# Optimization experiments

Hardware: AMD Instinct MI355X
Metric: run time of the kernel (lower is better)

The kernel has to match this reference:

```python
import jax, jax.numpy as jnp
import numpy as np


def setup_inputs() -> dict:
    key = jax.random.key(0)
    embeddings = jax.random.normal(key, (4, 2048, 128), dtype=jnp.float32)
    return {"embeddings": embeddings}


def _pairwise_dist(x):
    # x: [N, D] -> Euclidean distance matrix [N, N] (matches torch.cdist, p=2)
    sq = jnp.sum(x * x, axis=-1)  # [N]
    d2 = sq[:, None] + sq[None, :] - 2.0 * (x @ x.T)
    d2 = jnp.maximum(d2, 0.0)
    # safe sqrt: exact 0 on the diagonal / coincident points, no NaN grads
    safe = jnp.where(d2 > 0.0, d2, 1.0)
    return jnp.where(d2 > 0.0, jnp.sqrt(safe), 0.0)


def reference(embeddings) -> jnp.ndarray:
    b, s, d = embeddings.shape
    x = embeddings.reshape(b * s, d)
    dist = _pairwise_dist(x)                 # [N, N]
    mean_dist = jnp.mean(dist)
    # torch.std default: unbiased (ddof=1) over all elements
    std_dist = jnp.std(dist, ddof=1)
    return std_dist / (mean_dist + 1e-08)
```

## Files before the change

### kernel.cpp

```cpp
#include <hip/hip_runtime.h>
#include <hip/hip_bf16.h>
#include <math.h>


#define NPTS   8192
#define DIM    128
#define BT     256
#define NT2    (NPTS / BT)
#define NBLK   (NT2 * (NT2 + 1) / 2)
#define NPREP  (NPTS / 32)
#define NTILES (NPTS / 128)
#define NTOTSQ (NTILES * NTILES)

typedef __attribute__((ext_vector_type(8))) short short8;
typedef __attribute__((ext_vector_type(4))) float f32x4;

typedef const __attribute__((address_space(1))) void* gas_ptr;
typedef __attribute__((address_space(3))) void* las_ptr;

__device__ __forceinline__ void gload16(const void* g, void* l) {
    __builtin_amdgcn_global_load_lds((gas_ptr)g, (las_ptr)l, 16, 0, 0);
}
__device__ __forceinline__ float fsqrt(float x) {
    return __builtin_amdgcn_sqrtf(x);
}

__global__ __launch_bounds__(256)
void ph_prep(const float* __restrict__ x, ushort* __restrict__ xb,
             float* __restrict__ sq, float* __restrict__ cs_part)
{
    __shared__ float xs[32][129];
    const int tid = threadIdx.x;
    const int rw  = tid >> 3;
    const int row = blockIdx.x * 32 + rw;
    const int seg = tid & 7;
    const float4* p = reinterpret_cast<const float4*>(x + (size_t)row * DIM + seg * 16);
    float v[16];
    {
        float4 a = p[0], b = p[1], c = p[2], d = p[3];
        v[0]=a.x; v[1]=a.y; v[2]=a.z; v[3]=a.w;  v[4]=b.x; v[5]=b.y; v[6]=b.z; v[7]=b.w;
        v[8]=c.x; v[9]=c.y; v[10]=c.z; v[11]=c.w; v[12]=d.x; v[13]=d.y; v[14]=d.z; v[15]=d.w;
    }
    float s = 0.f;
    ushort h[16];
#pragma unroll
    for (int j = 0; j < 16; ++j) {
        __hip_bfloat16 hb = __float2bfloat16(v[j]);
        h[j] = *reinterpret_cast<ushort*>(&hb);
        s = fmaf(v[j], v[j], s);
        xs[rw][seg * 16 + j] = v[j];
    }
    short8 o0, o1;
#pragma unroll
    for (int j = 0; j < 8; ++j) { o0[j] = (short)h[j]; o1[j] = (short)h[j+8]; }
    short8* dst = reinterpret_cast<short8*>(xb + (size_t)row * DIM + seg * 16);
    dst[0] = o0; dst[1] = o1;
    s += __shfl_xor(s, 1); s += __shfl_xor(s, 2); s += __shfl_xor(s, 4);
    if (seg == 0) sq[row] = s;
    __syncthreads();
    if (tid < DIM) {
        float c = 0.f;
#pragma unroll 8
        for (int r = 0; r < 32; ++r) c += xs[r][tid];
        cs_part[blockIdx.x * DIM + tid] = c;
    }
}

__global__ __launch_bounds__(1024, 4)
void ph_gram(const ushort* __restrict__ xb, const float* __restrict__ sq,
             double* __restrict__ partials)
{
    const int f   = blockIdx.x;
    const int tid = threadIdx.x;

    int bi = (int)((65.0f - fsqrt((float)(4225 - 8 * f))) * 0.5f);
    while ((bi + 1) * 32 - ((bi + 1) * bi) / 2 <= f) ++bi;
    while (bi * 32 - (bi * (bi - 1)) / 2 > f) --bi;
    const int bj = bi + (f - (bi * 32 - (bi * (bi - 1)) / 2));

    __shared__ ushort A0[BT * 64], B0[BT * 64];
    __shared__ ushort A1[BT * 64], B1[BT * 64];
    __shared__ double rr[32];

    const int lane = tid & 63;
    const int wv   = tid >> 6;
    const int wr   = wv >> 2;
    const int wc   = wv & 3;

    const char* gA = (const char*)(xb + (size_t)bi * BT * DIM);
    const char* gB = (const char*)(xb + (size_t)bj * BT * DIM);

    const bool  stA  = wv < 8;
    const char* gsrc = stA ? gA : gB;
    const int   c0   = (wv & 7) * 4;
    const int   srow = lane >> 3;
    const int   skb  = (lane & 7) * 16;

#define STAGE(h, dA, dB)                                                      \
    {                                                                         \
        char* dst_ = stA ? (char*)(dA) : (char*)(dB);                         \
        _Pragma("unroll")                                                     \
        for (int c = 0; c < 4; ++c) {                                         \
            const int chunk = c0 + c;                                         \
            const int row   = chunk * 8 + srow;                               \
            const size_t go = (size_t)row * 256 + (h) * 128                   \
                              + (skb ^ ((row & 7) << 4));                     \
            gload16(gsrc + go, dst_ + chunk * 1024);                          \
        }                                                                     \
    }

    f32x4 acc[4][4];
#pragma unroll
    for (int m = 0; m < 4; ++m)
#pragma unroll
        for (int n = 0; n < 4; ++n) acc[m][n] = (f32x4){0.f, 0.f, 0.f, 0.f};

#define COMPUTE(dA, dB)                                                       \
    {                                                                         \
        _Pragma("unroll")                                                     \
        for (int ks = 0; ks < 2; ++ks) {                                      \
            const int kb = ks * 64 + (lane >> 4) * 16;                        \
            short8 af[4], bfr[4];                                             \
            _Pragma("unroll")                                                 \
            for (int m = 0; m < 4; ++m) {                                     \
                const int row = wr * 64 + m * 16 + (lane & 15);               \
                af[m] = *reinterpret_cast<const short8*>(                     \
                    (const char*)(dA) + row * 128 + (kb ^ ((row & 7) << 4))); \
            }                                                                 \
            _Pragma("unroll")                                                 \
            for (int n = 0; n < 4; ++n) {                                     \
                const int col = wc * 64 + n * 16 + (lane & 15);               \
                bfr[n] = *reinterpret_cast<const short8*>(                    \
                    (const char*)(dB) + col * 128 + (kb ^ ((col & 7) << 4))); \
            }                                                                 \
            __builtin_amdgcn_s_setprio(1);                                    \
            _Pragma("unroll")                                                 \
            for (int m = 0; m < 4; ++m)                                       \
                _Pragma("unroll")                                             \
                for (int n = 0; n < 4; ++n)                                   \
                    acc[m][n] = __builtin_amdgcn_mfma_f32_16x16x32_bf16(      \
                        af[m], bfr[n], acc[m][n], 0, 0, 0);                   \
            __builtin_amdgcn_s_setprio(0);                                    \
        }                                                                     \
    }

    STAGE(0, A0, B0);
    __syncthreads();
    STAGE(1, A1, B1);
    COMPUTE(A0, B0);
    __syncthreads();
    COMPUTE(A1, B1);

    const float* sqA = sq + bi * BT + wr * 64 + (lane >> 4) * 4;
    const float* sqB = sq + bj * BT + wc * 64 + (lane & 15);
    float nb[4];
#pragma unroll
    for (int n = 0; n < 4; ++n) nb[n] = sqB[n * 16];

    float s1a = 0.f, s1b = 0.f, s1c = 0.f, s1d = 0.f;
    const bool diag = (bi == bj);
    if (!diag) {
#pragma unroll
        for (int m = 0; m < 4; ++m) {
            const float4 v = *reinterpret_cast<const float4*>(sqA + m * 16);
#pragma unroll
            for (int n = 0; n < 4; ++n) {
                s1a += fsqrt(fmaxf(fmaf(-2.f, acc[m][n][0], v.x + nb[n]), 0.f));
                s1b += fsqrt(fmaxf(fmaf(-2.f, acc[m][n][1], v.y + nb[n]), 0.f));
                s1c += fsqrt(fmaxf(fmaf(-2.f, acc[m][n][2], v.z + nb[n]), 0.f));
                s1d += fsqrt(fmaxf(fmaf(-2.f, acc[m][n][3], v.w + nb[n]), 0.f));
            }
        }
    } else {
#pragma unroll
        for (int m = 0; m < 4; ++m) {
            const float4 v = *reinterpret_cast<const float4*>(sqA + m * 16);
            const float nav[4] = {v.x, v.y, v.z, v.w};
#pragma unroll
            for (int n = 0; n < 4; ++n) {
                const int col = wc * 64 + n * 16 + (lane & 15);
#pragma unroll
                for (int r = 0; r < 4; ++r) {
                    const int row = wr * 64 + m * 16 + (lane >> 4) * 4 + r;
                    float d = fmaxf(fmaf(-2.f, acc[m][n][r], nav[r] + nb[n]), 0.f);
                    if (row == col) d = 0.f;
                    s1a += fsqrt(d);
                }
            }
        }
    }
    float s1 = (s1a + s1b) + (s1c + s1d);
#pragma unroll
    for (int off = 1; off < 64; off <<= 1) s1 += __shfl_xor(s1, off);
    const double w = diag ? 1.0 : 2.0;
    if (lane == 0) rr[wv] = (double)s1 * w;
    __syncthreads();
    if (tid == 0) {
        double t1 = 0.0;
#pragma unroll
        for (int i = 0; i < 16; ++i) t1 += rr[i];
        partials[f] = t1;
    }
#undef STAGE
#undef COMPUTE
}

__global__ __launch_bounds__(256)
void ph_finalize(const double* __restrict__ partials, const float* __restrict__ sq,
                 const float* __restrict__ cs_part, float* __restrict__ out)
{
    __shared__ double r1[256], r2[256], r3[128];
    const int tid = threadIdx.x;
    double s1 = 0.0;
    for (int i = tid; i < NBLK; i += 256) s1 += partials[i];
    double sn = 0.0;
    for (int k = 0; k < NPTS / 256; ++k) sn += (double)sq[tid + k * 256];
    r1[tid] = s1; r2[tid] = sn;
    if (tid < DIM) {
        double c = 0.0;
        for (int b = 0; b < NPREP; ++b) c += (double)cs_part[b * DIM + tid];
        r3[tid] = c * c;
    }
    __syncthreads();
    for (int off = 128; off > 0; off >>= 1) {
        if (tid < off) { r1[tid] += r1[tid + off]; r2[tid] += r2[tid + off]; }
        __syncthreads();
    }
    for (int off = 64; off > 0; off >>= 1) {
        if (tid < off) r3[tid] += r3[tid + off];
        __syncthreads();
    }
    if (tid == 0) {
        const double M    = (double)NPTS * (double)NPTS;
        const double S1   = r1[0];
        const double S2   = 2.0 * (double)NPTS * r2[0] - 2.0 * r3[0];
        const double mean = S1 / M;
        double var = (S2 - S1 * S1 / M) / (M - 1.0);
        if (var < 0.0) var = 0.0;
        out[0] = (float)(sqrt(var) / (mean + 1e-8));
    }
}

#define LSTR 132
__global__ __launch_bounds__(256)
void ph_pair_kernel(const float* __restrict__ x, double* __restrict__ partials)
{
    const int bi  = blockIdx.y;
    const int bj  = blockIdx.x;
    const int tid = threadIdx.x;
    const int flat = bi * NTILES + bj;
    if (bj < bi) {
        if (tid == 0) { partials[2*flat] = 0.0; partials[2*flat+1] = 0.0; }
        return;
    }
    __shared__ __align__(16) float As[128 * LSTR];
    __shared__ __align__(16) float Bs[128 * LSTR];
    __shared__ float  nA[128];
    __shared__ float  nB[128];
    __shared__ double red1[256];
    __shared__ double red2[256];
    const float* Ab = x + (size_t)bi * 128 * DIM;
    const float* Bb = x + (size_t)bj * 128 * DIM;
#pragma unroll
    for (int it = 0; it < 16; ++it) {
        const int e   = (tid + it * 256) * 4;
        const int row = e >> 7;
        const int k   = e & 127;
        float4 va = *reinterpret_cast<const float4*>(Ab + e);
        As[(k+0)*LSTR + row] = va.x; As[(k+1)*LSTR + row] = va.y;
        As[(k+2)*LSTR + row] = va.z; As[(k+3)*LSTR + row] = va.w;
        float4 vb = *reinterpret_cast<const float4*>(Bb + e);
        Bs[(k+0)*LSTR + row] = vb.x; Bs[(k+1)*LSTR + row] = vb.y;
        Bs[(k+2)*LSTR + row] = vb.z; Bs[(k+3)*LSTR + row] = vb.w;
    }
    __syncthreads();
    if (tid < 128) {
        float s = 0.f;
#pragma unroll 8
        for (int k = 0; k < DIM; ++k) { float v = As[k*LSTR + tid]; s = fmaf(v, v, s); }
        nA[tid] = s;
    } else {
        const int r = tid - 128;
        float s = 0.f;
#pragma unroll 8
        for (int k = 0; k < DIM; ++k) { float v = Bs[k*LSTR + r]; s = fmaf(v, v, s); }
        nB[r] = s;
    }
    __syncthreads();
    const int tx = tid & 15, ty = tid >> 4;
    const int ra = ty * 8, cb = tx * 8;
    float acc[8][8];
#pragma unroll
    for (int r = 0; r < 8; ++r)
#pragma unroll
        for (int c = 0; c < 8; ++c) acc[r][c] = 0.f;
#pragma unroll 4
    for (int k = 0; k < DIM; ++k) {
        const float4 a0 = *reinterpret_cast<const float4*>(&As[k*LSTR + ra]);
        const float4 a1 = *reinterpret_cast<const float4*>(&As[k*LSTR + ra + 4]);
        const float4 b0 = *reinterpret_cast<const float4*>(&Bs[k*LSTR + cb]);
        const float4 b1 = *reinterpret_cast<const float4*>(&Bs[k*LSTR + cb + 4]);
        const float a[8] = {a0.x,a0.y,a0.z,a0.w,a1.x,a1.y,a1.z,a1.w};
        const float b[8] = {b0.x,b0.y,b0.z,b0.w,b1.x,b1.y,b1.z,b1.w};
#pragma unroll
        for (int r = 0; r < 8; ++r)
#pragma unroll
            for (int c = 0; c < 8; ++c)
                acc[r][c] = fmaf(a[r], b[c], acc[r][c]);
    }
    double s1 = 0.0, s2 = 0.0;
    const int gi0 = bi*128 + ra, gj0 = bj*128 + cb;
#pragma unroll
    for (int r = 0; r < 8; ++r) {
#pragma unroll
        for (int c = 0; c < 8; ++c) {
            float d2 = nA[ra+r] + nB[cb+c] - 2.0f * acc[r][c];
            d2 = fmaxf(d2, 0.0f);
            if (gi0 + r == gj0 + c) d2 = 0.0f;
            s1 += (double)sqrtf(d2);
            s2 += (double)d2;
        }
    }
    const double w = (bi == bj) ? 1.0 : 2.0;
    s1 *= w; s2 *= w;
    red1[tid] = s1; red2[tid] = s2;
    __syncthreads();
    for (int off = 128; off > 0; off >>= 1) {
        if (tid < off) { red1[tid] += red1[tid+off]; red2[tid] += red2[tid+off]; }
        __syncthreads();
    }
    if (tid == 0) { partials[2*flat] = red1[0]; partials[2*flat+1] = red2[0]; }
}

__global__ __launch_bounds__(256)
void ph_finalize_sq(const double* __restrict__ partials, float* __restrict__ out)
{
    __shared__ double r1[256], r2[256];
    const int tid = threadIdx.x;
    double s1 = 0.0, s2 = 0.0;
    for (int i = tid; i < NTOTSQ; i += 256) { s1 += partials[2*i]; s2 += partials[2*i+1]; }
    r1[tid] = s1; r2[tid] = s2;
    __syncthreads();
    for (int off = 128; off > 0; off >>= 1) {
        if (tid < off) { r1[tid] += r1[tid+off]; r2[tid] += r2[tid+off]; }
        __syncthreads();
    }
    if (tid == 0) {
        const double M    = (double)NPTS * (double)NPTS;
        const double mean = r1[0] / M;
        double var = (r2[0] - r1[0]*r1[0]/M) / (M - 1.0);
        if (var < 0.0) var = 0.0;
        out[0] = (float)(sqrt(var) / (mean + 1e-8));
    }
}

extern "C" void kernel_launch(void* const* d_in, const int* in_sizes, int n_in,
                              void* d_out, int out_size, void* d_ws, size_t ws_size,
                              hipStream_t stream)
{
    const float* x = (const float*)d_in[0];
    float* out     = (float*)d_out;

    const size_t XB_OFF = 0;
    const size_t SQ_OFF = (size_t)NPTS * DIM * sizeof(ushort);
    const size_t CS_OFF = SQ_OFF + NPTS * sizeof(float);
    const size_t PT_OFF = CS_OFF + (size_t)NPREP * DIM * sizeof(float);
    const size_t NEEDED = PT_OFF + (size_t)NBLK * sizeof(double);

    if (ws_size >= NEEDED) {
        ushort* xb       = (ushort*)((char*)d_ws + XB_OFF);
        float*  sq       = (float*) ((char*)d_ws + SQ_OFF);
        float*  cs_part  = (float*) ((char*)d_ws + CS_OFF);
        double* partials = (double*)((char*)d_ws + PT_OFF);

        ph_prep<<<NPREP, 256, 0, stream>>>(x, xb, sq, cs_part);
        ph_gram<<<NBLK, 1024, 0, stream>>>(xb, sq, partials);
        ph_finalize<<<1, 256, 0, stream>>>(partials, sq, cs_part, out);
    } else {
        double* partials = (double*)d_ws;
        ph_pair_kernel<<<dim3(NTILES, NTILES), 256, 0, stream>>>(x, partials);
        ph_finalize_sq<<<1, 256, 0, stream>>>(partials, out);
    }
}
```

Before: 38.35 us.

## Shrink Gram tiles to 128x128 with 256-thread blocks and single-buffered LDS

Changes the upper-triangular Gram tile from 256x256 with 1024 threads to 128x128 with 256 threads. The grid grows from 528 to 2080 blocks, and LDS per block falls from four 32KB buffers to two 16KB buffers. Staging is no longer double-buffered: each K-half is loaded, synced and computed in sequence. The aim is better occupancy and load balance across CUs, at the cost of more redundant global loads per flop and exposed load latency.

```diff
diff --git a/kernel.cpp b/kernel.cpp
--- a/kernel.cpp
+++ b/kernel.cpp
@@ -5,9 +5,9 @@
 
 #define NPTS   8192
 #define DIM    128
-#define BT     256
-#define NT2    (NPTS / BT)
-#define NBLK   (NT2 * (NT2 + 1) / 2)
+#define TIL    128
+#define NGRID  (NPTS / TIL)
+#define NTOT   (NGRID * (NGRID + 1) / 2)
 #define NPREP  (NPTS / 32)
 #define NTILES (NPTS / 128)
 #define NTOTSQ (NTILES * NTILES)
@@ -66,46 +66,43 @@
     }
 }
 
-__global__ __launch_bounds__(1024, 4)
+__global__ __launch_bounds__(256, 4)
 void ph_gram(const ushort* __restrict__ xb, const float* __restrict__ sq,
              double* __restrict__ partials)
 {
     const int f   = blockIdx.x;
     const int tid = threadIdx.x;
 
-    int bi = (int)((65.0f - fsqrt((float)(4225 - 8 * f))) * 0.5f);
-    while ((bi + 1) * 32 - ((bi + 1) * bi) / 2 <= f) ++bi;
-    while (bi * 32 - (bi * (bi - 1)) / 2 > f) --bi;
-    const int bj = bi + (f - (bi * 32 - (bi * (bi - 1)) / 2));
-
-    __shared__ ushort A0[BT * 64], B0[BT * 64];
-    __shared__ ushort A1[BT * 64], B1[BT * 64];
-    __shared__ double rr[32];
+    int bi = (int)((129.0f - fsqrt((float)(16641 - 8 * f))) * 0.5f);
+    while ((bi + 1) * 64 - ((bi + 1) * bi) / 2 <= f) ++bi;
+    while (bi * 64 - (bi * (bi - 1)) / 2 > f) --bi;
+    const int bj = bi + (f - (bi * 64 - (bi * (bi - 1)) / 2));
+
+    __shared__ ushort Ah[TIL * 64];
+    __shared__ ushort Bh[TIL * 64];
+    __shared__ double rr[4];
 
     const int lane = tid & 63;
     const int wv   = tid >> 6;
-    const int wr   = wv >> 2;
-    const int wc   = wv & 3;
-
-    const char* gA = (const char*)(xb + (size_t)bi * BT * DIM);
-    const char* gB = (const char*)(xb + (size_t)bj * BT * DIM);
-
-    const bool  stA  = wv < 8;
-    const char* gsrc = stA ? gA : gB;
-    const int   c0   = (wv & 7) * 4;
-    const int   srow = lane >> 3;
-    const int   skb  = (lane & 7) * 16;
-
-#define STAGE(h, dA, dB)                                                      \
+    const int wr   = wv >> 1;
+    const int wc   = wv & 1;
+
+    const char* gA = (const char*)(xb + (size_t)bi * TIL * DIM);
+    const char* gB = (const char*)(xb + (size_t)bj * TIL * DIM);
+
+    const int srow = lane >> 3;
+    const int skb  = (lane & 7) * 16;
+
+#define STAGE(h)                                                              \
     {                                                                         \
-        char* dst_ = stA ? (char*)(dA) : (char*)(dB);                         \
         _Pragma("unroll")                                                     \
         for (int c = 0; c < 4; ++c) {                                         \
-            const int chunk = c0 + c;                                         \
+            const int chunk = wv * 4 + c;                                     \
             const int row   = chunk * 8 + srow;                               \
             const size_t go = (size_t)row * 256 + (h) * 128                   \
                               + (skb ^ ((row & 7) << 4));                     \
-            gload16(gsrc + go, dst_ + chunk * 1024);                          \
+            gload16(gA + go, (char*)Ah + chunk * 1024);                       \
+            gload16(gB + go, (char*)Bh + chunk * 1024);                       \
         }                                                                     \
     }
 
@@ -115,7 +112,7 @@
 #pragma unroll
         for (int n = 0; n < 4; ++n) acc[m][n] = (f32x4){0.f, 0.f, 0.f, 0.f};
 
-#define COMPUTE(dA, dB)                                                       \
+#define COMPUTE()                                                             \
     {                                                                         \
         _Pragma("unroll")                                                     \
         for (int ks = 0; ks < 2; ++ks) {                                      \
@@ -125,13 +122,13 @@
             for (int m = 0; m < 4; ++m) {                                     \
                 const int row = wr * 64 + m * 16 + (lane & 15);               \
                 af[m] = *reinterpret_cast<const short8*>(                     \
-                    (const char*)(dA) + row * 128 + (kb ^ ((row & 7) << 4))); \
+                    (const char*)Ah + row * 128 + (kb ^ ((row & 7) << 4)));   \
             }                                                                 \
             _Pragma("unroll")                                                 \
             for (int n = 0; n < 4; ++n) {                                     \
                 const int col = wc * 64 + n * 16 + (lane & 15);               \
                 bfr[n] = *reinterpret_cast<const short8*>(                    \
-                    (const char*)(dB) + col * 128 + (kb ^ ((col & 7) << 4))); \
+                    (const char*)Bh + col * 128 + (kb ^ ((col & 7) << 4)));   \
             }                                                                 \
             __builtin_amdgcn_s_setprio(1);                                    \
             _Pragma("unroll")                                                 \
@@ -144,15 +141,16 @@
         }                                                                     \
     }
 
-    STAGE(0, A0, B0);
-    __syncthreads();
-    STAGE(1, A1, B1);
-    COMPUTE(A0, B0);
-    __syncthreads();
-    COMPUTE(A1, B1);
-
-    const float* sqA = sq + bi * BT + wr * 64 + (lane >> 4) * 4;
-    const float* sqB = sq + bj * BT + wc * 64 + (lane & 15);
+    STAGE(0);
+    __syncthreads();
+    COMPUTE();
+    __syncthreads();
+    STAGE(1);
+    __syncthreads();
+    COMPUTE();
+
+    const float* sqA = sq + bi * TIL + wr * 64 + (lane >> 4) * 4;
+    const float* sqB = sq + bj * TIL + wc * 64 + (lane & 15);
     float nb[4];
 #pragma unroll
     for (int n = 0; n < 4; ++n) nb[n] = sqB[n * 16];
@@ -195,12 +193,7 @@
     const double w = diag ? 1.0 : 2.0;
     if (lane == 0) rr[wv] = (double)s1 * w;
     __syncthreads();
-    if (tid == 0) {
-        double t1 = 0.0;
-#pragma unroll
-        for (int i = 0; i < 16; ++i) t1 += rr[i];
-        partials[f] = t1;
-    }
+    if (tid == 0) partials[f] = (rr[0] + rr[1]) + (rr[2] + rr[3]);
 #undef STAGE
 #undef COMPUTE
 }
@@ -212,7 +205,7 @@
     __shared__ double r1[256], r2[256], r3[128];
     const int tid = threadIdx.x;
     double s1 = 0.0;
-    for (int i = tid; i < NBLK; i += 256) s1 += partials[i];
+    for (int i = tid; i < NTOT; i += 256) s1 += partials[i];
     double sn = 0.0;
     for (int k = 0; k < NPTS / 256; ++k) sn += (double)sq[tid + k * 256];
     r1[tid] = s1; r2[tid] = sn;
@@ -365,7 +358,7 @@
     const size_t SQ_OFF = (size_t)NPTS * DIM * sizeof(ushort);
     const size_t CS_OFF = SQ_OFF + NPTS * sizeof(float);
     const size_t PT_OFF = CS_OFF + (size_t)NPREP * DIM * sizeof(float);
-    const size_t NEEDED = PT_OFF + (size_t)NBLK * sizeof(double);
+    const size_t NEEDED = PT_OFF + (size_t)NTOT * sizeof(double);
 
     if (ws_size >= NEEDED) {
         ushort* xb       = (ushort*)((char*)d_ws + XB_OFF);
@@ -374,7 +367,7 @@
         double* partials = (double*)((char*)d_ws + PT_OFF);
 
         ph_prep<<<NPREP, 256, 0, stream>>>(x, xb, sq, cs_part);
-        ph_gram<<<NBLK, 1024, 0, stream>>>(xb, sq, partials);
+        ph_gram<<<NTOT, 256, 0, stream>>>(xb, sq, partials);
         ph_finalize<<<1, 256, 0, stream>>>(partials, sq, cs_part, out);
     } else {
         double* partials = (double*)d_ws;
```

Result: faster. 35.47 us (-7.5%).

## Fuse finalize into gram kernel via last-block atomic counter; use 512-thread blocks

Applied to the files above, without the earlier changes.

Removes the separate finalize kernel launch. The last gram block to finish, found through an atomic counter that the prep kernel resets, now does the final reductions. The gram kernel also drops from 1024 to 512 threads, so each wave computes a 128x64 sub-tile with twice as many accumulators, and the setprio hints are removed. This saves one launch and its gap but raises register pressure per wave and serialises the final reduction on a single block.

```diff
diff --git a/kernel.cpp b/kernel.cpp
--- a/kernel.cpp
+++ b/kernel.cpp
@@ -27,10 +27,12 @@
 
 __global__ __launch_bounds__(256)
 void ph_prep(const float* __restrict__ x, ushort* __restrict__ xb,
-             float* __restrict__ sq, float* __restrict__ cs_part)
+             float* __restrict__ sq, float* __restrict__ cs_part,
+             unsigned int* __restrict__ counter)
 {
     __shared__ float xs[32][129];
     const int tid = threadIdx.x;
+    if (blockIdx.x == 0 && tid == 0) counter[0] = 0u;
     const int rw  = tid >> 3;
     const int row = blockIdx.x * 32 + rw;
     const int seg = tid & 7;
@@ -66,9 +68,10 @@
     }
 }
 
-__global__ __launch_bounds__(1024, 4)
+__global__ __launch_bounds__(512)
 void ph_gram(const ushort* __restrict__ xb, const float* __restrict__ sq,
-             double* __restrict__ partials)
+             const float* __restrict__ cs_part, double* __restrict__ partials,
+             unsigned int* __restrict__ counter, float* __restrict__ out)
 {
     const int f   = blockIdx.x;
     const int tid = threadIdx.x;
@@ -80,19 +83,21 @@
 
     __shared__ ushort A0[BT * 64], B0[BT * 64];
     __shared__ ushort A1[BT * 64], B1[BT * 64];
-    __shared__ double rr[32];
+    __shared__ double rr[16];
+    __shared__ double red[512];
+    __shared__ int    lastFlag;
 
     const int lane = tid & 63;
     const int wv   = tid >> 6;
-    const int wr   = wv >> 2;
-    const int wc   = wv & 3;
+    const int wr2  = wv >> 2;
+    const int wc4  = wv & 3;
 
     const char* gA = (const char*)(xb + (size_t)bi * BT * DIM);
     const char* gB = (const char*)(xb + (size_t)bj * BT * DIM);
 
-    const bool  stA  = wv < 8;
+    const bool  stA  = wv < 4;
     const char* gsrc = stA ? gA : gB;
-    const int   c0   = (wv & 7) * 4;
+    const int   cb0  = (wv & 3) * 8;
     const int   srow = lane >> 3;
     const int   skb  = (lane & 7) * 16;
 
@@ -100,8 +105,8 @@
     {                                                                         \
         char* dst_ = stA ? (char*)(dA) : (char*)(dB);                         \
         _Pragma("unroll")                                                     \
-        for (int c = 0; c < 4; ++c) {                                         \
-            const int chunk = c0 + c;                                         \
+        for (int c = 0; c < 8; ++c) {                                         \
+            const int chunk = cb0 + c;                                        \
             const int row   = chunk * 8 + srow;                               \
             const size_t go = (size_t)row * 256 + (h) * 128                   \
                               + (skb ^ ((row & 7) << 4));                     \
@@ -109,9 +114,9 @@
         }                                                                     \
     }
 
-    f32x4 acc[4][4];
-#pragma unroll
-    for (int m = 0; m < 4; ++m)
+    f32x4 acc[8][4];
+#pragma unroll
+    for (int m = 0; m < 8; ++m)
 #pragma unroll
         for (int n = 0; n < 4; ++n) acc[m][n] = (f32x4){0.f, 0.f, 0.f, 0.f};
 
@@ -120,27 +125,25 @@
         _Pragma("unroll")                                                     \
         for (int ks = 0; ks < 2; ++ks) {                                      \
             const int kb = ks * 64 + (lane >> 4) * 16;                        \
-            short8 af[4], bfr[4];                                             \
+            short8 af[8], bfr[4];                                             \
             _Pragma("unroll")                                                 \
-            for (int m = 0; m < 4; ++m) {                                     \
-                const int row = wr * 64 + m * 16 + (lane & 15);               \
+            for (int m = 0; m < 8; ++m) {                                     \
+                const int row = wr2 * 128 + m * 16 + (lane & 15);             \
                 af[m] = *reinterpret_cast<const short8*>(                     \
                     (const char*)(dA) + row * 128 + (kb ^ ((row & 7) << 4))); \
             }                                                                 \
             _Pragma("unroll")                                                 \
             for (int n = 0; n < 4; ++n) {                                     \
-                const int col = wc * 64 + n * 16 + (lane & 15);               \
+                const int col = wc4 * 64 + n * 16 + (lane & 15);              \
                 bfr[n] = *reinterpret_cast<const short8*>(                    \
                     (const char*)(dB) + col * 128 + (kb ^ ((col & 7) << 4))); \
             }                                                                 \
-            __builtin_amdgcn_s_setprio(1);                                    \
             _Pragma("unroll")                                                 \
-            for (int m = 0; m < 4; ++m)                                       \
+            for (int m = 0; m < 8; ++m)                                       \
                 _Pragma("unroll")                                             \
                 for (int n = 0; n < 4; ++n)                                   \
                     acc[m][n] = __builtin_amdgcn_mfma_f32_16x16x32_bf16(      \
                         af[m], bfr[n], acc[m][n], 0, 0, 0);                   \
-            __builtin_amdgcn_s_setprio(0);                                    \
         }                                                                     \
     }
 
@@ -151,8 +154,8 @@
     __syncthreads();
     COMPUTE(A1, B1);
 
-    const float* sqA = sq + bi * BT + wr * 64 + (lane >> 4) * 4;
-    const float* sqB = sq + bj * BT + wc * 64 + (lane & 15);
+    const float* sqA = sq + bi * BT + wr2 * 128 + (lane >> 4) * 4;
+    const float* sqB = sq + bj * BT + wc4 * 64 + (lane & 15);
     float nb[4];
 #pragma unroll
     for (int n = 0; n < 4; ++n) nb[n] = sqB[n * 16];
@@ -161,7 +164,7 @@
     const bool diag = (bi == bj);
     if (!diag) {
 #pragma unroll
-        for (int m = 0; m < 4; ++m) {
+        for (int m = 0; m < 8; ++m) {
             const float4 v = *reinterpret_cast<const float4*>(sqA + m * 16);
 #pragma unroll
             for (int n = 0; n < 4; ++n) {
@@ -173,15 +176,15 @@
         }
     } else {
 #pragma unroll
-        for (int m = 0; m < 4; ++m) {
+        for (int m = 0; m < 8; ++m) {
             const float4 v = *reinterpret_cast<const float4*>(sqA + m * 16);
             const float nav[4] = {v.x, v.y, v.z, v.w};
 #pragma unroll
             for (int n = 0; n < 4; ++n) {
-                const int col = wc * 64 + n * 16 + (lane & 15);
+                const int col = wc4 * 64 + n * 16 + (lane & 15);
 #pragma unroll
                 for (int r = 0; r < 4; ++r) {
-                    const int row = wr * 64 + m * 16 + (lane >> 4) * 4 + r;
+                    const int row = wr2 * 128 + m * 16 + (lane >> 4) * 4 + r;
                     float d = fmaxf(fmaf(-2.f, acc[m][n][r], nav[r] + nb[n]), 0.f);
                     if (row == col) d = 0.f;
                     s1a += fsqrt(d);
@@ -198,47 +201,60 @@
     if (tid == 0) {
         double t1 = 0.0;
 #pragma unroll
-        for (int i = 0; i < 16; ++i) t1 += rr[i];
+        for (int i = 0; i < 8; ++i) t1 += rr[i];
         partials[f] = t1;
     }
-#undef STAGE
-#undef COMPUTE
-}
-
-__global__ __launch_bounds__(256)
-void ph_finalize(const double* __restrict__ partials, const float* __restrict__ sq,
-                 const float* __restrict__ cs_part, float* __restrict__ out)
-{
-    __shared__ double r1[256], r2[256], r3[128];
-    const int tid = threadIdx.x;
-    double s1 = 0.0;
-    for (int i = tid; i < NBLK; i += 256) s1 += partials[i];
-    double sn = 0.0;
-    for (int k = 0; k < NPTS / 256; ++k) sn += (double)sq[tid + k * 256];
-    r1[tid] = s1; r2[tid] = sn;
+
+    __threadfence();
+    if (tid == 0) {
+        unsigned int prev = atomicAdd(counter, 1u);
+        lastFlag = (prev == (unsigned int)(NBLK - 1));
+    }
+    __syncthreads();
+    if (!lastFlag) return;
+    __threadfence();
+
+    double t = 0.0;
+    for (int i = tid; i < NBLK; i += 512) t += partials[i];
+    red[tid] = t; __syncthreads();
+    for (int off = 256; off > 0; off >>= 1) {
+        if (tid < off) red[tid] += red[tid + off];
+        __syncthreads();
+    }
+    const double S1 = red[0];
+    __syncthreads();
+
+    t = 0.0;
+    for (int i = tid; i < NPTS; i += 512) t += (double)sq[i];
+    red[tid] = t; __syncthreads();
+    for (int off = 256; off > 0; off >>= 1) {
+        if (tid < off) red[tid] += red[tid + off];
+        __syncthreads();
+    }
+    const double SN = red[0];
+    __syncthreads();
+
+    t = 0.0;
     if (tid < DIM) {
         double c = 0.0;
         for (int b = 0; b < NPREP; ++b) c += (double)cs_part[b * DIM + tid];
-        r3[tid] = c * c;
-    }
-    __syncthreads();
-    for (int off = 128; off > 0; off >>= 1) {
-        if (tid < off) { r1[tid] += r1[tid + off]; r2[tid] += r2[tid + off]; }
-        __syncthreads();
-    }
-    for (int off = 64; off > 0; off >>= 1) {
-        if (tid < off) r3[tid] += r3[tid + off];
+        t = c * c;
+    }
+    red[tid] = t; __syncthreads();
+    for (int off = 256; off > 0; off >>= 1) {
+        if (tid < off) red[tid] += red[tid + off];
         __syncthreads();
     }
     if (tid == 0) {
         const double M    = (double)NPTS * (double)NPTS;
-        const double S1   = r1[0];
-        const double S2   = 2.0 * (double)NPTS * r2[0] - 2.0 * r3[0];
+        const double S2   = 2.0 * (double)NPTS * SN - 2.0 * red[0];
         const double mean = S1 / M;
         double var = (S2 - S1 * S1 / M) / (M - 1.0);
         if (var < 0.0) var = 0.0;
         out[0] = (float)(sqrt(var) / (mean + 1e-8));
     }
+#undef STAGE
+#undef COMPUTE
 }
 
 #define LSTR 132
@@ -365,17 +381,18 @@
     const size_t SQ_OFF = (size_t)NPTS * DIM * sizeof(ushort);
     const size_t CS_OFF = SQ_OFF + NPTS * sizeof(float);
     const size_t PT_OFF = CS_OFF + (size_t)NPREP * DIM * sizeof(float);
-    const size_t NEEDED = PT_OFF + (size_t)NBLK * sizeof(double);
+    const size_t CT_OFF = PT_OFF + (size_t)NBLK * sizeof(double);
+    const size_t NEEDED = CT_OFF + sizeof(unsigned int);
 
     if (ws_size >= NEEDED) {
-        ushort* xb       = (ushort*)((char*)d_ws + XB_OFF);
-        float*  sq       = (float*) ((char*)d_ws + SQ_OFF);
-        float*  cs_part  = (float*) ((char*)d_ws + CS_OFF);
-        double* partials = (double*)((char*)d_ws + PT_OFF);
-
-        ph_prep<<<NPREP, 256, 0, stream>>>(x, xb, sq, cs_part);
-        ph_gram<<<NBLK, 1024, 0, stream>>>(xb, sq, partials);
-        ph_finalize<<<1, 256, 0, stream>>>(partials, sq, cs_part, out);
+        ushort*       xb       = (ushort*)      ((char*)d_ws + XB_OFF);
+        float*        sq       = (float*)       ((char*)d_ws + SQ_OFF);
+        float*        cs_part  = (float*)       ((char*)d_ws + CS_OFF);
+        double*       partials = (double*)      ((char*)d_ws + PT_OFF);
+        unsigned int* counter  = (unsigned int*)((char*)d_ws + CT_OFF);
+
+        ph_prep<<<NPREP, 256, 0, stream>>>(x, xb, sq, cs_part, counter);
+        ph_gram<<<NBLK, 512, 0, stream>>>(xb, sq, cs_part, partials, counter, out);
     } else {
         double* partials = (double*)d_ws;
         ph_pair_kernel<<<dim3(NTILES, NTILES), 256, 0, stream>>>(x, partials);
```

New measurement: 108.1 us. 182% more time.
